# Kernel tuning notes

Measured on AMD Instinct MI355X. Metric: run time of the kernel, lower is better.

## Reference

```python
import jax, jax.numpy as jnp
import numpy as np

N = 50000      # nodes
E = 800000     # edges (before self loops)
F = 128        # node_feat_dim
HID = 128      # hidden_dim
LN_EPS = 1e-5
NEG_SLOPE = 0.2


def setup_inputs() -> dict:
    key = jax.random.key(0)
    ks = jax.random.split(key, 32)
    g = lambda k, shape, s=0.05: jax.random.normal(k, shape, dtype=jnp.float32) * s
    inp = {}
    inp["x"] = jax.random.normal(ks[0], (N, F), dtype=jnp.float32)
    inp["edge_index"] = jax.random.randint(ks[1], (2, E), 0, N)
    i = 2
    # conv1: F -> 4 heads x 32, concat -> HID
    inp["W1l"] = g(ks[i], (F, HID)); inp["b1l"] = jnp.zeros((HID,), jnp.float32)
    inp["W1r"] = g(ks[i+1], (F, HID)); inp["b1r"] = jnp.zeros((HID,), jnp.float32)
    inp["a1"] = g(ks[i+2], (4, HID // 4)); inp["c1"] = jnp.zeros((HID,), jnp.float32)
    inp["g1"] = jnp.ones((HID,), jnp.float32); inp["be1"] = jnp.zeros((HID,), jnp.float32)
    # conv2: HID -> 4 heads x 32, concat -> HID
    inp["W2l"] = g(ks[i+3], (HID, HID)); inp["b2l"] = jnp.zeros((HID,), jnp.float32)
    inp["W2r"] = g(ks[i+4], (HID, HID)); inp["b2r"] = jnp.zeros((HID,), jnp.float32)
    inp["a2"] = g(ks[i+5], (4, HID // 4)); inp["c2"] = jnp.zeros((HID,), jnp.float32)
    inp["g2"] = jnp.ones((HID,), jnp.float32); inp["be2"] = jnp.zeros((HID,), jnp.float32)
    # conv3: HID -> 1 head x HID, mean -> HID
    inp["W3l"] = g(ks[i+6], (HID, HID)); inp["b3l"] = jnp.zeros((HID,), jnp.float32)
    inp["W3r"] = g(ks[i+7], (HID, HID)); inp["b3r"] = jnp.zeros((HID,), jnp.float32)
    inp["a3"] = g(ks[i+8], (1, HID)); inp["c3"] = jnp.zeros((HID,), jnp.float32)
    inp["g3"] = jnp.ones((HID,), jnp.float32); inp["be3"] = jnp.zeros((HID,), jnp.float32)
    return inp


def _gatv2(x, Wl, bl, Wr, br, att, bias, src, dst, heads, outc, concat):
    """GATv2Conv: xl=source transform, xr=target transform, edge-wise
    LeakyReLU attention, per-destination segment softmax, scatter-add."""
    n = x.shape[0]
    xl = (x @ Wl + bl).reshape(n, heads, outc)   # lin_l -> source (x_j)
    e_feat = jax.nn.leaky_relu(xl[src] + ((x @ Wr + br).reshape(n, heads, outc))[dst], NEG_SLOPE)  # [E,H,C]
    logits = jnp.einsum('ehc,hc->eh', e_feat, att)                 # [E,H]
    m = jax.ops.segment_max(logits, dst, num_segments=n)           # [N,H]
    a = jnp.exp(logits - m[dst])
    denom = jax.ops.segment_sum(a, dst, num_segments=n)            # [N,H]
    a = a / denom[dst]
    out = jax.ops.segment_sum(xl[src] * a[:, :, None], dst, num_segments=n)  # [N,H,C]
    out = out.reshape(n, heads * outc) if concat else out.mean(axis=1)
    return out + bias


def _ln(h, g, b):
    mu = h.mean(-1, keepdims=True)
    var = ((h - mu) ** 2).mean(-1, keepdims=True)
    return (h - mu) * jax.lax.rsqrt(var + LN_EPS) * g + b


def reference(x, edge_index,
              W1l, b1l, W1r, b1r, a1, c1, g1, be1,
              W2l, b2l, W2r, b2r, a2, c2, g2, be2,
              W3l, b3l, W3r, b3r, a3, c3, g3, be3):
    n = x.shape[0]
    loops = jnp.arange(n, dtype=edge_index.dtype)
    src = jnp.concatenate([edge_index[0], loops])  # add_self_loops=True
    dst = jnp.concatenate([edge_index[1], loops])
    h = _gatv2(x, W1l, b1l, W1r, b1r, a1, c1, src, dst, 4, HID // 4, True)
    h = jax.nn.relu(_ln(h, g1, be1))  # dropout is identity in eval
    h = _gatv2(h, W2l, b2l, W2r, b2r, a2, c2, src, dst, 4, HID // 4, True)
    h = jax.nn.relu(_ln(h, g2, be2))
    h = _gatv2(h, W3l, b3l, W3r, b3r, a3, c3, src, dst, 1, HID, False)
    h = jax.nn.relu(_ln(h, g3, be3))
    return h
```

## Files before the change

### kernel.cpp

```cpp
#include <hip/hip_runtime.h>
#include <hip/hip_bf16.h>


typedef __attribute__((ext_vector_type(8))) short bf16x8;
typedef __attribute__((ext_vector_type(4))) float f32x4;
typedef __attribute__((ext_vector_type(2))) float f32x2;

#define CAP 64

__device__ __forceinline__ ushort f2bf(float f) {
    unsigned u = __float_as_uint(f);
    unsigned r = (u + 0x7fffu + ((u >> 16) & 1u)) >> 16;
    return (ushort)r;
}
__device__ __forceinline__ f32x2 up2(unsigned u) {
    f32x2 r;
    r[0] = __uint_as_float(u << 16);
    r[1] = __uint_as_float(u & 0xffff0000u);
    return r;
}


__global__ __launch_bounds__(256) void prep_kernel(
    const float* __restrict__ x, ushort* __restrict__ xb, int n4,
    const float* W0, const float* W1, const float* W2,
    const float* W3, const float* W4, const float* W5,
    ushort* __restrict__ WT, int* __restrict__ cursor, int nzb, int n) {
    __shared__ ushort s[128 * 129];
    int tid = threadIdx.x;
    if (blockIdx.x < 6) {
        const float* Ws[6] = {W0, W1, W2, W3, W4, W5};
        const float* W = Ws[blockIdx.x];
        ushort* O = WT + blockIdx.x * 16384;
        for (int r = 0; r < 128; r += 2) {
            int k = r + (tid >> 7);
            int nn = tid & 127;
            s[nn * 129 + k] = f2bf(W[k * 128 + nn]);
        }
        __syncthreads();
        for (int i = tid; i < 16384; i += 256) {
            int nn = i >> 7, k = i & 127;
            O[i] = s[nn * 129 + k];
        }
    } else if (blockIdx.x < 6 + nzb) {
        int base = (blockIdx.x - 6) * 1024 + tid * 4;
        if (base + 3 < n) {
            *(int4*)&cursor[base] = make_int4(0, 0, 0, 0);
        } else {
            for (int j = 0; j < 4; ++j)
                if (base + j < n) cursor[base + j] = 0;
        }
    } else {
        int i = (blockIdx.x - 6 - nzb) * 256 + tid;
        if (i >= n4) return;
        float4 v = ((const float4*)x)[i];
        ushort4 o;
        o.x = f2bf(v.x); o.y = f2bf(v.y); o.z = f2bf(v.z); o.w = f2bf(v.w);
        ((ushort4*)xb)[i] = o;
    }
}


__global__ __launch_bounds__(256) void scatter_part_kernel(
    const int* __restrict__ srcrow, const int* __restrict__ dstrow,
    int E, int n, int* __restrict__ cursor, int* __restrict__ srcs) {
    int part = blockIdx.x & 7;
    int sub = blockIdx.x >> 3;
    int nsub = gridDim.x >> 3;
    int ppn = (n + 7) / 8;
    int lo = part * ppn;
    int hi = lo + ppn; if (hi > n) hi = n;
    int ET = E + n;
    int chunk = (ET + nsub - 1) / nsub;
    int s0 = sub * chunk, s1 = s0 + chunk; if (s1 > ET) s1 = ET;
    for (int i = s0 + threadIdx.x; i < s1; i += 256) {
        int d = (i < E) ? dstrow[i] : (i - E);
        if (d >= lo && d < hi) {
            int s = (i < E) ? srcrow[i] : (i - E);
            int pos = atomicAdd(&cursor[d], 1);
            if (pos < CAP) srcs[(d << 6) + pos] = s << 8;
        }
    }
}


__global__ __launch_bounds__(256) void dual_gemm_mfma(
    const ushort* __restrict__ A,
    const ushort* __restrict__ WTl, const ushort* __restrict__ WTr,
    const float* __restrict__ bl, const float* __restrict__ br,
    ushort* __restrict__ XL, ushort* __restrict__ XR, int n) {
    int tid = threadIdx.x;
    int wid = tid >> 6, lane = tid & 63;
    int ln15 = lane & 15, hi = lane >> 4;
    int row0 = blockIdx.x * 64;

    const ushort* WT  = (wid < 2) ? WTl : WTr;
    const float* bias = (wid < 2) ? bl : br;
    ushort* OUT       = (wid < 2) ? XL : XR;
    int colbase = (wid & 1) * 64;

    float bv[4];
    #pragma unroll
    for (int nn = 0; nn < 4; ++nn) bv[nn] = bias[colbase + nn * 16 + ln15];

    f32x4 acc[4][4];
    #pragma unroll
    for (int m = 0; m < 4; ++m)
        #pragma unroll
        for (int nn = 0; nn < 4; ++nn) acc[m][nn] = (f32x4){0.f, 0.f, 0.f, 0.f};

    #pragma unroll
    for (int kk = 0; kk < 4; ++kk) {
        int kb = kk * 64 + hi * 16;
        bf16x8 a[4], b[4];
        #pragma unroll
        for (int m = 0; m < 4; ++m) {
            int r = row0 + m * 16 + ln15;
            a[m] = *(const bf16x8*)((const char*)A + (size_t)r * 256 + kb);
        }
        #pragma unroll
        for (int nn = 0; nn < 4; ++nn) {
            int c = colbase + nn * 16 + ln15;
            b[nn] = *(const bf16x8*)((const char*)WT + (size_t)c * 256 + kb);
        }
        #pragma unroll
        for (int m = 0; m < 4; ++m)
            #pragma unroll
            for (int nn = 0; nn < 4; ++nn)
                acc[m][nn] = __builtin_amdgcn_mfma_f32_16x16x32_bf16(a[m], b[nn], acc[m][nn], 0, 0, 0);
    }

    #pragma unroll
    for (int m = 0; m < 4; ++m) {
        int rbase = row0 + m * 16 + hi * 4;
        bool full = (rbase + 3 < n);
        #pragma unroll
        for (int nn = 0; nn < 4; ++nn) {
            int c = colbase + nn * 16 + ln15;
            ushort* o = OUT + (size_t)rbase * 128 + c;
            float b = bv[nn];
            __hip_bfloat162 h01 = __float22bfloat162_rn(make_float2(acc[m][nn][0] + b, acc[m][nn][1] + b));
            __hip_bfloat162 h23 = __float22bfloat162_rn(make_float2(acc[m][nn][2] + b, acc[m][nn][3] + b));
            ushort2 u01 = *(ushort2*)&h01;
            ushort2 u23 = *(ushort2*)&h23;
            if (full) {
                o[0] = u01.x; o[128] = u01.y; o[256] = u23.x; o[384] = u23.y;
            } else {
                if (rbase + 0 < n) o[0]   = u01.x;
                if (rbase + 1 < n) o[128] = u01.y;
                if (rbase + 2 < n) o[256] = u23.x;
                if (rbase + 3 < n) o[384] = u23.y;
            }
        }
    }
}


template <int GS>
__device__ __forceinline__ void edge_op(uint4 U, const f32x2* xr, const f32x2* at,
                                        f32x2* acc, float& den) {
    f32x2 a0 = up2(U.x), a1 = up2(U.y), a2 = up2(U.z), a3 = up2(U.w);
    f32x2 t = a0 + xr[0];
    t = __builtin_elementwise_max(t, t * 0.2f);
    f32x2 dd = t * at[0];
    t = a1 + xr[1];
    t = __builtin_elementwise_max(t, t * 0.2f);
    dd = __builtin_elementwise_fma(t, at[1], dd);
    t = a2 + xr[2];
    t = __builtin_elementwise_max(t, t * 0.2f);
    dd = __builtin_elementwise_fma(t, at[2], dd);
    t = a3 + xr[3];
    t = __builtin_elementwise_max(t, t * 0.2f);
    dd = __builtin_elementwise_fma(t, at[3], dd);
    float p = dd[0] + dd[1];
    #pragma unroll
    for (int d = 1; d < GS; d <<= 1) p += __shfl_xor(p, d, 64);
    float ew = exp2f(p);
    f32x2 ev; ev[0] = ew; ev[1] = ew;
    acc[0] = __builtin_elementwise_fma(ev, a0, acc[0]);
    acc[1] = __builtin_elementwise_fma(ev, a1, acc[1]);
    acc[2] = __builtin_elementwise_fma(ev, a2, acc[2]);
    acc[3] = __builtin_elementwise_fma(ev, a3, acc[3]);
    den += ew;
}


__global__ __launch_bounds__(256) void agg_head_kernel(
    const ushort* __restrict__ XL, const ushort* __restrict__ XR,
    const int* __restrict__ deg, const int* __restrict__ srcs,
    const float* __restrict__ att, const float* __restrict__ bias,
    ushort* __restrict__ OUT, int n) {
    int b = blockIdx.x;
    int head = (b & 7) >> 1;
    int s = ((b >> 3) << 1) | (b & 1);
    int nsub = (gridDim.x >> 3) << 1;
    int tid = threadIdx.x;
    int wid = tid >> 6, lane = tid & 63;
    int ng = lane >> 2;
    int l4 = lane & 3;
    int hb = head * 64 + l4 * 16;
    int c0 = head * 32 + l4 * 8;

    const char* XLc = (const char*)XL;

    f32x2 at[4];
    {
        const float4* ap = (const float4*)(att + c0);
        float4 a0 = ap[0], a1 = ap[1];
        at[0][0] = a0.x; at[0][1] = a0.y; at[1][0] = a0.z; at[1][1] = a0.w;
        at[2][0] = a1.x; at[2][1] = a1.y; at[3][0] = a1.z; at[3][1] = a1.w;
        #pragma unroll
        for (int j = 0; j < 4; ++j) at[j] = at[j] * 1.44269504f;
    }
    f32x2 bi[4];
    {
        const f32x2* bp = (const f32x2*)(bias + c0);
        #pragma unroll
        for (int j = 0; j < 4; ++j) bi[j] = bp[j];
    }

    int npb = (n + nsub - 1) / nsub;
    int v0 = s * npb;
    int v1 = v0 + npb; if (v1 > n) v1 = n;

    for (int base = v0; base < v1; base += 64) {
        int node = base + wid * 16 + ng;
        bool alive = (node < v1);

        f32x2 xr[4];
        int e = 0;
        const int* sp = srcs;
        if (alive) {
            uint4 ur = *(const uint4*)((const char*)XR + ((size_t)node << 8) + hb);
            xr[0] = up2(ur.x); xr[1] = up2(ur.y); xr[2] = up2(ur.z); xr[3] = up2(ur.w);
            e = deg[node]; if (e > CAP) e = CAP;
            sp = srcs + ((size_t)node << 6);
        } else {
            #pragma unroll
            for (int j = 0; j < 4; ++j) { xr[j][0] = 0.f; xr[j][1] = 0.f; }
        }

        f32x2 acc[4];
        #pragma unroll
        for (int j = 0; j < 4; ++j) { acc[j][0] = 0.f; acc[j][1] = 0.f; }
        float den = 0.f;

        int i = 0;
        for (; i + 4 <= e; i += 4) {
            int4 ofs = *(const int4*)(sp + i);
            uint4 u0 = *(const uint4*)(XLc + ofs.x + hb);
            uint4 u1 = *(const uint4*)(XLc + ofs.y + hb);
            uint4 u2 = *(const uint4*)(XLc + ofs.z + hb);
            uint4 u3 = *(const uint4*)(XLc + ofs.w + hb);
            edge_op<4>(u0, xr, at, acc, den);
            edge_op<4>(u1, xr, at, acc, den);
            edge_op<4>(u2, xr, at, acc, den);
            edge_op<4>(u3, xr, at, acc, den);
        }
        for (; i < e; ++i) {
            uint4 u0 = *(const uint4*)(XLc + sp[i] + hb);
            edge_op<4>(u0, xr, at, acc, den);
        }

        if (alive) {
            float inv = 1.f / den;
            f32x2 iv; iv[0] = inv; iv[1] = inv;
            uint4 ov;
            unsigned* op = (unsigned*)&ov;
            #pragma unroll
            for (int j = 0; j < 4; ++j) {
                f32x2 o = __builtin_elementwise_fma(acc[j], iv, bi[j]);
                __hip_bfloat162 h = __float22bfloat162_rn(make_float2(o[0], o[1]));
                op[j] = *(unsigned*)&h;
            }
            *(uint4*)((char*)OUT + ((size_t)node << 8) + hb) = ov;
        }
    }
}


__global__ __launch_bounds__(256) void ln_relu_kernel(
    ushort* __restrict__ H, const float* __restrict__ gamma,
    const float* __restrict__ beta, int n) {
    int tid = threadIdx.x;
    int wid = tid >> 6, lane = tid & 63;
    int node = blockIdx.x * 16 + wid * 4 + (lane >> 4);
    int l = lane & 15, c0 = l * 8;
    bool alive = (node < n);

    f32x2 o[4];
    if (alive) {
        uint4 u = *(const uint4*)&H[(size_t)node * 128 + c0];
        o[0] = up2(u.x); o[1] = up2(u.y); o[2] = up2(u.z); o[3] = up2(u.w);
    } else {
        #pragma unroll
        for (int j = 0; j < 4; ++j) { o[j][0] = 0.f; o[j][1] = 0.f; }
    }

    float ssum = 0.f;
    #pragma unroll
    for (int j = 0; j < 4; ++j) ssum += o[j][0] + o[j][1];
    #pragma unroll
    for (int d = 1; d < 16; d <<= 1) ssum += __shfl_xor(ssum, d, 64);
    float mu = ssum * (1.f / 128.f);
    float vsum = 0.f;
    #pragma unroll
    for (int j = 0; j < 4; ++j) {
        float d0 = o[j][0] - mu, d1 = o[j][1] - mu;
        vsum += d0 * d0 + d1 * d1;
    }
    #pragma unroll
    for (int d = 1; d < 16; d <<= 1) vsum += __shfl_xor(vsum, d, 64);
    float rstd = rsqrtf(vsum * (1.f / 128.f) + 1e-5f);

    if (!alive) return;

    const f32x2* gp = (const f32x2*)(gamma + c0);
    const f32x2* ep = (const f32x2*)(beta + c0);
    uint4 ov;
    unsigned* op = (unsigned*)&ov;
    #pragma unroll
    for (int j = 0; j < 4; ++j) {
        f32x2 gj = gp[j], bj = ep[j];
        float y0 = fmaxf(fmaf((o[j][0] - mu) * rstd, gj[0], bj[0]), 0.f);
        float y1 = fmaxf(fmaf((o[j][1] - mu) * rstd, gj[1], bj[1]), 0.f);
        __hip_bfloat162 h = __float22bfloat162_rn(make_float2(y0, y1));
        op[j] = *(unsigned*)&h;
    }
    *(uint4*)&H[(size_t)node * 128 + c0] = ov;
}


template <int H, bool OUT_BF16>
__global__ __launch_bounds__(256) void aggregate_kernel(
    const ushort* __restrict__ XL, const ushort* __restrict__ XR,
    const int* __restrict__ deg, const int* __restrict__ srcs,
    const float* __restrict__ att, const float* __restrict__ bias,
    const float* __restrict__ gamma, const float* __restrict__ beta,
    void* __restrict__ OUTP, int n) {
    int tid = threadIdx.x;
    int wid = tid >> 6, lane = tid & 63;
    int g = lane >> 4, l = lane & 15;
    int node = blockIdx.x * 16 + wid * 4 + g;
    bool alive = (node < n);
    int c0 = l * 8;
    constexpr int GS = (128 / H) / 8;

    const char* XLc = (const char*)XL;
    int lb = l * 16;

    f32x2 at[4];
    {
        const float4* ap = (const float4*)(att + c0);
        float4 a0 = ap[0], a1 = ap[1];
        at[0][0] = a0.x; at[0][1] = a0.y; at[1][0] = a0.z; at[1][1] = a0.w;
        at[2][0] = a1.x; at[2][1] = a1.y; at[3][0] = a1.z; at[3][1] = a1.w;
        #pragma unroll
        for (int j = 0; j < 4; ++j) at[j] = at[j] * 1.44269504f;
    }

    f32x2 xr[4];
    int e = 0;
    const int* sp = srcs;
    if (alive) {
        uint4 ur = *(const uint4*)((const char*)XR + ((size_t)node << 8) + lb);
        xr[0] = up2(ur.x); xr[1] = up2(ur.y); xr[2] = up2(ur.z); xr[3] = up2(ur.w);
        e = deg[node]; if (e > CAP) e = CAP;
        sp = srcs + ((size_t)node << 6);
    } else {
        #pragma unroll
        for (int j = 0; j < 4; ++j) { xr[j][0] = 0.f; xr[j][1] = 0.f; }
    }

    f32x2 acc[4];
    #pragma unroll
    for (int j = 0; j < 4; ++j) { acc[j][0] = 0.f; acc[j][1] = 0.f; }
    float den = 0.f;

    int i = 0;
    for (; i + 4 <= e; i += 4) {
        int4 ofs = *(const int4*)(sp + i);
        uint4 u0 = *(const uint4*)(XLc + ofs.x + lb);
        uint4 u1 = *(const uint4*)(XLc + ofs.y + lb);
        uint4 u2 = *(const uint4*)(XLc + ofs.z + lb);
        uint4 u3 = *(const uint4*)(XLc + ofs.w + lb);
        edge_op<GS>(u0, xr, at, acc, den);
        edge_op<GS>(u1, xr, at, acc, den);
        edge_op<GS>(u2, xr, at, acc, den);
        edge_op<GS>(u3, xr, at, acc, den);
    }
    for (; i < e; ++i) {
        uint4 u0 = *(const uint4*)(XLc + sp[i] + lb);
        edge_op<GS>(u0, xr, at, acc, den);
    }

    float inv = 1.f / den;
    f32x2 o[4];
    {
        const f32x2* bp = (const f32x2*)(bias + c0);
        f32x2 iv; iv[0] = inv; iv[1] = inv;
        #pragma unroll
        for (int j = 0; j < 4; ++j) o[j] = __builtin_elementwise_fma(acc[j], iv, bp[j]);
    }

    float ssum = 0.f;
    #pragma unroll
    for (int j = 0; j < 4; ++j) ssum += o[j][0] + o[j][1];
    #pragma unroll
    for (int d = 1; d < 16; d <<= 1) ssum += __shfl_xor(ssum, d, 64);
    float mu = ssum * (1.f / 128.f);
    float vsum = 0.f;
    #pragma unroll
    for (int j = 0; j < 4; ++j) {
        float d0 = o[j][0] - mu, d1 = o[j][1] - mu;
        vsum += d0 * d0 + d1 * d1;
    }
    #pragma unroll
    for (int d = 1; d < 16; d <<= 1) vsum += __shfl_xor(vsum, d, 64);
    float rstd = rsqrtf(vsum * (1.f / 128.f) + 1e-5f);

    if (!alive) return;

    const f32x2* gp = (const f32x2*)(gamma + c0);
    const f32x2* ep = (const f32x2*)(beta + c0);
    float y[8];
    #pragma unroll
    for (int j = 0; j < 4; ++j) {
        f32x2 gj = gp[j], bj = ep[j];
        y[2 * j]     = fmaxf(fmaf((o[j][0] - mu) * rstd, gj[0], bj[0]), 0.f);
        y[2 * j + 1] = fmaxf(fmaf((o[j][1] - mu) * rstd, gj[1], bj[1]), 0.f);
    }

    if (OUT_BF16) {
        __hip_bfloat162 h0 = __float22bfloat162_rn(make_float2(y[0], y[1]));
        __hip_bfloat162 h1 = __float22bfloat162_rn(make_float2(y[2], y[3]));
        __hip_bfloat162 h2 = __float22bfloat162_rn(make_float2(y[4], y[5]));
        __hip_bfloat162 h3 = __float22bfloat162_rn(make_float2(y[6], y[7]));
        uint4 ov;
        ov.x = *(unsigned*)&h0; ov.y = *(unsigned*)&h1;
        ov.z = *(unsigned*)&h2; ov.w = *(unsigned*)&h3;
        *(uint4*)&((ushort*)OUTP)[(size_t)node * 128 + c0] = ov;
    } else {
        float* O = (float*)OUTP + (size_t)node * 128 + c0;
        *(float4*)O = make_float4(y[0], y[1], y[2], y[3]);
        *(float4*)(O + 4) = make_float4(y[4], y[5], y[6], y[7]);
    }
}


extern "C" void kernel_launch(void* const* d_in, const int* in_sizes, int n_in,
                              void* d_out, int out_size, void* d_ws, size_t ws_size,
                              hipStream_t stream) {
    const float* x  = (const float*)d_in[0];
    const int*   ei = (const int*)d_in[1];
    const float *W1l = (const float*)d_in[2],  *b1l = (const float*)d_in[3];
    const float *W1r = (const float*)d_in[4],  *b1r = (const float*)d_in[5];
    const float *a1  = (const float*)d_in[6],  *c1  = (const float*)d_in[7];
    const float *g1  = (const float*)d_in[8],  *be1 = (const float*)d_in[9];
    const float *W2l = (const float*)d_in[10], *b2l = (const float*)d_in[11];
    const float *W2r = (const float*)d_in[12], *b2r = (const float*)d_in[13];
    const float *a2  = (const float*)d_in[14], *c2  = (const float*)d_in[15];
    const float *g2  = (const float*)d_in[16], *be2 = (const float*)d_in[17];
    const float *W3l = (const float*)d_in[18], *b3l = (const float*)d_in[19];
    const float *W3r = (const float*)d_in[20], *b3r = (const float*)d_in[21];
    const float *a3  = (const float*)d_in[22], *c3  = (const float*)d_in[23];
    const float *g3  = (const float*)d_in[24], *be3 = (const float*)d_in[25];

    int n  = in_sizes[0] / 128;
    int E  = in_sizes[1] / 2;
    size_t nPad = (size_t)((n + 63) / 64) * 64;

    char* ws = (char*)d_ws;
    ushort* xb = (ushort*)ws;                      ws += nPad * 128 * 2;
    ushort* XL = (ushort*)ws;                      ws += nPad * 128 * 2;
    ushort* XR = (ushort*)ws;                      ws += nPad * 128 * 2;
    ushort* hb = (ushort*)ws;                      ws += nPad * 128 * 2;
    ushort* WT = (ushort*)ws;                      ws += 6 * 16384 * 2;
    int* cursor = (int*)ws;                        ws += (size_t)n * 4;
    int* srcs   = (int*)ws;

    const int* srcrow = ei;
    const int* dstrow = ei + E;

    int n4 = n * 128 / 4;
    int nzb = (n + 1023) / 1024;
    prep_kernel<<<6 + nzb + (n4 + 255) / 256, 256, 0, stream>>>(
        x, xb, n4, W1l, W1r, W2l, W2r, W3l, W3r, WT, cursor, nzb, n);

    scatter_part_kernel<<<2048, 256, 0, stream>>>(srcrow, dstrow, E, n, cursor, srcs);

    int gb = (int)(nPad / 64);
    int ab = (n + 15) / 16;

    dual_gemm_mfma<<<gb, 256, 0, stream>>>(xb, WT + 0 * 16384, WT + 1 * 16384, b1l, b1r, XL, XR, n);
    agg_head_kernel<<<2048, 256, 0, stream>>>(XL, XR, cursor, srcs, a1, c1, hb, n);
    ln_relu_kernel<<<ab, 256, 0, stream>>>(hb, g1, be1, n);
    dual_gemm_mfma<<<gb, 256, 0, stream>>>(hb, WT + 2 * 16384, WT + 3 * 16384, b2l, b2r, XL, XR, n);
    agg_head_kernel<<<2048, 256, 0, stream>>>(XL, XR, cursor, srcs, a2, c2, hb, n);
    ln_relu_kernel<<<ab, 256, 0, stream>>>(hb, g2, be2, n);
    dual_gemm_mfma<<<gb, 256, 0, stream>>>(hb, WT + 4 * 16384, WT + 5 * 16384, b3l, b3r, XL, XR, n);
    aggregate_kernel<1, false><<<ab, 256, 0, stream>>>(XL, XR, cursor, srcs, a3, c3, g3, be3, d_out, n);
}
```

Measured before the change: 413.5 us.

## Store XL/XR in head-major slices for contiguous per-head gathers

Measured after the change: 407.3 us. No clear change (-1.5%).

```diff
diff --git a/kernel.cpp b/kernel.cpp
--- a/kernel.cpp
+++ b/kernel.cpp
@@ -78,7 +78,7 @@
         if (d >= lo && d < hi) {
             int s = (i < E) ? srcrow[i] : (i - E);
             int pos = atomicAdd(&cursor[d], 1);
-            if (pos < CAP) srcs[(d << 6) + pos] = s << 8;
+            if (pos < CAP) srcs[(d << 6) + pos] = s << 6;
         }
     }
 }
@@ -88,7 +88,7 @@
     const ushort* __restrict__ A,
     const ushort* __restrict__ WTl, const ushort* __restrict__ WTr,
     const float* __restrict__ bl, const float* __restrict__ br,
-    ushort* __restrict__ XL, ushort* __restrict__ XR, int n) {
+    ushort* __restrict__ XL, ushort* __restrict__ XR, int n, int sliceE) {
     int tid = threadIdx.x;
     int wid = tid >> 6, lane = tid & 63;
     int ln15 = lane & 15, hi = lane >> 4;
@@ -136,20 +136,22 @@
         bool full = (rbase + 3 < n);
         #pragma unroll
         for (int nn = 0; nn < 4; ++nn) {
-            int c = colbase + nn * 16 + ln15;
-            ushort* o = OUT + (size_t)rbase * 128 + c;
+            int c = colbase + nn * 16;
+            int head = c >> 5;
+            ushort* o = OUT + (size_t)head * sliceE + (size_t)rbase * 32
+                            + (nn & 1) * 16 + ln15;
             float b = bv[nn];
             __hip_bfloat162 h01 = __float22bfloat162_rn(make_float2(acc[m][nn][0] + b, acc[m][nn][1] + b));
             __hip_bfloat162 h23 = __float22bfloat162_rn(make_float2(acc[m][nn][2] + b, acc[m][nn][3] + b));
             ushort2 u01 = *(ushort2*)&h01;
             ushort2 u23 = *(ushort2*)&h23;
             if (full) {
-                o[0] = u01.x; o[128] = u01.y; o[256] = u23.x; o[384] = u23.y;
+                o[0] = u01.x; o[32] = u01.y; o[64] = u23.x; o[96] = u23.y;
             } else {
-                if (rbase + 0 < n) o[0]   = u01.x;
-                if (rbase + 1 < n) o[128] = u01.y;
-                if (rbase + 2 < n) o[256] = u23.x;
-                if (rbase + 3 < n) o[384] = u23.y;
+                if (rbase + 0 < n) o[0]  = u01.x;
+                if (rbase + 1 < n) o[32] = u01.y;
+                if (rbase + 2 < n) o[64] = u23.x;
+                if (rbase + 3 < n) o[96] = u23.y;
             }
         }
     }
@@ -189,7 +191,7 @@
     const ushort* __restrict__ XL, const ushort* __restrict__ XR,
     const int* __restrict__ deg, const int* __restrict__ srcs,
     const float* __restrict__ att, const float* __restrict__ bias,
-    ushort* __restrict__ OUT, int n) {
+    ushort* __restrict__ OUT, int n, int sliceB) {
     int b = blockIdx.x;
     int head = (b & 7) >> 1;
     int s = ((b >> 3) << 1) | (b & 1);
@@ -198,10 +200,10 @@
     int wid = tid >> 6, lane = tid & 63;
     int ng = lane >> 2;
     int l4 = lane & 3;
-    int hb = head * 64 + l4 * 16;
     int c0 = head * 32 + l4 * 8;
 
-    const char* XLc = (const char*)XL;
+    const char* XLb = (const char*)XL + (size_t)head * sliceB + l4 * 16;
+    const char* XRb = (const char*)XR + (size_t)head * sliceB + l4 * 16;
 
     f32x2 at[4];
     {
@@ -231,7 +233,7 @@
         int e = 0;
         const int* sp = srcs;
         if (alive) {
-            uint4 ur = *(const uint4*)((const char*)XR + ((size_t)node << 8) + hb);
+            uint4 ur = *(const uint4*)(XRb + ((size_t)node << 6));
             xr[0] = up2(ur.x); xr[1] = up2(ur.y); xr[2] = up2(ur.z); xr[3] = up2(ur.w);
             e = deg[node]; if (e > CAP) e = CAP;
             sp = srcs + ((size_t)node << 6);
@@ -248,17 +250,17 @@
         int i = 0;
         for (; i + 4 <= e; i += 4) {
             int4 ofs = *(const int4*)(sp + i);
-            uint4 u0 = *(const uint4*)(XLc + ofs.x + hb);
-            uint4 u1 = *(const uint4*)(XLc + ofs.y + hb);
-            uint4 u2 = *(const uint4*)(XLc + ofs.z + hb);
-            uint4 u3 = *(const uint4*)(XLc + ofs.w + hb);
+            uint4 u0 = *(const uint4*)(XLb + ofs.x);
+            uint4 u1 = *(const uint4*)(XLb + ofs.y);
+            uint4 u2 = *(const uint4*)(XLb + ofs.z);
+            uint4 u3 = *(const uint4*)(XLb + ofs.w);
             edge_op<4>(u0, xr, at, acc, den);
             edge_op<4>(u1, xr, at, acc, den);
             edge_op<4>(u2, xr, at, acc, den);
             edge_op<4>(u3, xr, at, acc, den);
         }
         for (; i < e; ++i) {
-            uint4 u0 = *(const uint4*)(XLc + sp[i] + hb);
+            uint4 u0 = *(const uint4*)(XLb + sp[i]);
             edge_op<4>(u0, xr, at, acc, den);
         }
 
@@ -273,7 +275,7 @@
                 __hip_bfloat162 h = __float22bfloat162_rn(make_float2(o[0], o[1]));
                 op[j] = *(unsigned*)&h;
             }
-            *(uint4*)((char*)OUT + ((size_t)node << 8) + hb) = ov;
+            *(uint4*)((char*)OUT + ((size_t)node << 8) + c0 * 2) = ov;
         }
     }
 }
@@ -331,23 +333,21 @@
 }
 
 
-template <int H, bool OUT_BF16>
-__global__ __launch_bounds__(256) void aggregate_kernel(
+__global__ __launch_bounds__(256) void aggregate3_kernel(
     const ushort* __restrict__ XL, const ushort* __restrict__ XR,
     const int* __restrict__ deg, const int* __restrict__ srcs,
     const float* __restrict__ att, const float* __restrict__ bias,
     const float* __restrict__ gamma, const float* __restrict__ beta,
-    void* __restrict__ OUTP, int n) {
+    float* __restrict__ OUTP, int n, int sliceB) {
     int tid = threadIdx.x;
     int wid = tid >> 6, lane = tid & 63;
     int g = lane >> 4, l = lane & 15;
     int node = blockIdx.x * 16 + wid * 4 + g;
     bool alive = (node < n);
     int c0 = l * 8;
-    constexpr int GS = (128 / H) / 8;
-
-    const char* XLc = (const char*)XL;
-    int lb = l * 16;
+
+    const char* XLb = (const char*)XL + (size_t)(l >> 2) * sliceB + (l & 3) * 16;
+    const char* XRb = (const char*)XR + (size_t)(l >> 2) * sliceB + (l & 3) * 16;
 
     f32x2 at[4];
     {
@@ -363,7 +363,7 @@
     int e = 0;
     const int* sp = srcs;
     if (alive) {
-        uint4 ur = *(const uint4*)((const char*)XR + ((size_t)node << 8) + lb);
+        uint4 ur = *(const uint4*)(XRb + ((size_t)node << 6));
         xr[0] = up2(ur.x); xr[1] = up2(ur.y); xr[2] = up2(ur.z); xr[3] = up2(ur.w);
         e = deg[node]; if (e > CAP) e = CAP;
         sp = srcs + ((size_t)node << 6);
@@ -380,18 +380,18 @@
     int i = 0;
     for (; i + 4 <= e; i += 4) {
         int4 ofs = *(const int4*)(sp + i);
-        uint4 u0 = *(const uint4*)(XLc + ofs.x + lb);
-        uint4 u1 = *(const uint4*)(XLc + ofs.y + lb);
-        uint4 u2 = *(const uint4*)(XLc + ofs.z + lb);
-        uint4 u3 = *(const uint4*)(XLc + ofs.w + lb);
-        edge_op<GS>(u0, xr, at, acc, den);
-        edge_op<GS>(u1, xr, at, acc, den);
-        edge_op<GS>(u2, xr, at, acc, den);
-        edge_op<GS>(u3, xr, at, acc, den);
+        uint4 u0 = *(const uint4*)(XLb + ofs.x);
+        uint4 u1 = *(const uint4*)(XLb + ofs.y);
+        uint4 u2 = *(const uint4*)(XLb + ofs.z);
+        uint4 u3 = *(const uint4*)(XLb + ofs.w);
+        edge_op<16>(u0, xr, at, acc, den);
+        edge_op<16>(u1, xr, at, acc, den);
+        edge_op<16>(u2, xr, at, acc, den);
+        edge_op<16>(u3, xr, at, acc, den);
     }
     for (; i < e; ++i) {
-        uint4 u0 = *(const uint4*)(XLc + sp[i] + lb);
-        edge_op<GS>(u0, xr, at, acc, den);
+        uint4 u0 = *(const uint4*)(XLb + sp[i]);
+        edge_op<16>(u0, xr, at, acc, den);
     }
 
     float inv = 1.f / den;
@@ -431,20 +431,9 @@
         y[2 * j + 1] = fmaxf(fmaf((o[j][1] - mu) * rstd, gj[1], bj[1]), 0.f);
     }
 
-    if (OUT_BF16) {
-        __hip_bfloat162 h0 = __float22bfloat162_rn(make_float2(y[0], y[1]));
-        __hip_bfloat162 h1 = __float22bfloat162_rn(make_float2(y[2], y[3]));
-        __hip_bfloat162 h2 = __float22bfloat162_rn(make_float2(y[4], y[5]));
-        __hip_bfloat162 h3 = __float22bfloat162_rn(make_float2(y[6], y[7]));
-        uint4 ov;
-        ov.x = *(unsigned*)&h0; ov.y = *(unsigned*)&h1;
-        ov.z = *(unsigned*)&h2; ov.w = *(unsigned*)&h3;
-        *(uint4*)&((ushort*)OUTP)[(size_t)node * 128 + c0] = ov;
-    } else {
-        float* O = (float*)OUTP + (size_t)node * 128 + c0;
-        *(float4*)O = make_float4(y[0], y[1], y[2], y[3]);
-        *(float4*)(O + 4) = make_float4(y[4], y[5], y[6], y[7]);
-    }
+    float* O = OUTP + (size_t)node * 128 + c0;
+    *(float4*)O = make_float4(y[0], y[1], y[2], y[3]);
+    *(float4*)(O + 4) = make_float4(y[4], y[5], y[6], y[7]);
 }
 
 
@@ -469,6 +458,8 @@
     int n  = in_sizes[0] / 128;
     int E  = in_sizes[1] / 2;
     size_t nPad = (size_t)((n + 63) / 64) * 64;
+    int sliceE = (int)(nPad * 32);
+    int sliceB = (int)(nPad * 64);
 
     char* ws = (char*)d_ws;
     ushort* xb = (ushort*)ws;                      ws += nPad * 128 * 2;
@@ -492,12 +483,16 @@
     int gb = (int)(nPad / 64);
     int ab = (n + 15) / 16;
 
-    dual_gemm_mfma<<<gb, 256, 0, stream>>>(xb, WT + 0 * 16384, WT + 1 * 16384, b1l, b1r, XL, XR, n);
-    agg_head_kernel<<<2048, 256, 0, stream>>>(XL, XR, cursor, srcs, a1, c1, hb, n);
+    dual_gemm_mfma<<<gb, 256, 0, stream>>>(xb, WT + 0 * 16384, WT + 1 * 16384,
+                                           b1l, b1r, XL, XR, n, sliceE);
+    agg_head_kernel<<<2048, 256, 0, stream>>>(XL, XR, cursor, srcs, a1, c1, hb, n, sliceB);
     ln_relu_kernel<<<ab, 256, 0, stream>>>(hb, g1, be1, n);
-    dual_gemm_mfma<<<gb, 256, 0, stream>>>(hb, WT + 2 * 16384, WT + 3 * 16384, b2l, b2r, XL, XR, n);
-    agg_head_kernel<<<2048, 256, 0, stream>>>(XL, XR, cursor, srcs, a2, c2, hb, n);
+    dual_gemm_mfma<<<gb, 256, 0, stream>>>(hb, WT + 2 * 16384, WT + 3 * 16384,
+                                           b2l, b2r, XL, XR, n, sliceE);
+    agg_head_kernel<<<2048, 256, 0, stream>>>(XL, XR, cursor, srcs, a2, c2, hb, n, sliceB);
     ln_relu_kernel<<<ab, 256, 0, stream>>>(hb, g2, be2, n);
-    dual_gemm_mfma<<<gb, 256, 0, stream>>>(hb, WT + 4 * 16384, WT + 5 * 16384, b3l, b3r, XL, XR, n);
-    aggregate_kernel<1, false><<<ab, 256, 0, stream>>>(XL, XR, cursor, srcs, a3, c3, g3, be3, d_out, n);
-}
+    dual_gemm_mfma<<<gb, 256, 0, stream>>>(hb, WT + 4 * 16384, WT + 5 * 16384,
+                                           b3l, b3r, XL, XR, n, sliceE);
+    aggregate3_kernel<<<ab, 256, 0, stream>>>(XL, XR, cursor, srcs, a3, c3, g3, be3,
+                                              (float*)d_out, n, sliceB);
+}
```
